# Performance work log

Measured on AMD Instinct MI355X. Metric: run time of the kernel, lower is better.

## Reference

```python
import jax, jax.numpy as jnp
import numpy as np

EMBED_DIM = 768
OUT_DIM = 768
EPS = 1e-06


def setup_inputs() -> dict:
    key = jax.random.key(0)
    ks = jax.random.split(key, 7)
    s_in = 1.0 / np.sqrt(EMBED_DIM)
    x = jax.random.normal(ks[0], (32, 1024, EMBED_DIM), dtype=jnp.float32)
    Wq = jax.random.normal(ks[1], (OUT_DIM, EMBED_DIM), dtype=jnp.float32) * s_in
    bq = jax.random.normal(ks[2], (OUT_DIM,), dtype=jnp.float32) * 0.01
    Wk = jax.random.normal(ks[3], (OUT_DIM, EMBED_DIM), dtype=jnp.float32) * s_in
    bk = jax.random.normal(ks[4], (OUT_DIM,), dtype=jnp.float32) * 0.01
    Wv = jax.random.normal(ks[5], (OUT_DIM, EMBED_DIM), dtype=jnp.float32) * s_in
    bv = jax.random.normal(ks[6], (OUT_DIM,), dtype=jnp.float32) * 0.01
    return {"x": x, "Wq": Wq, "bq": bq, "Wk": Wk, "bk": bk, "Wv": Wv, "bv": bv}


def reference(x, Wq, bq, Wk, bk, Wv, bv):
    # Q/K/V projections: nn.Linear computes x @ W.T + b
    Q = jnp.einsum('bnd,od->bno', x, Wq) + bq  # [B, N, O]
    K = jnp.einsum('bnd,od->bno', x, Wk) + bk
    V = jnp.einsum('bnd,od->bno', x, Wv) + bv
    scale = jnp.sqrt(jnp.asarray(OUT_DIM, dtype=x.dtype)) + EPS
    attn = jnp.einsum('bqo,bko->bqk', Q, K) / scale  # [B, N, N]
    weights = jax.nn.softmax(attn, axis=-1)
    # dropout p=0.0 -> identity (eval/inference)
    return jnp.einsum('bqk,bko->bqo', weights, V)
```

## Files before the change

kernel.cpp:

```cpp
#include <hip/hip_runtime.h>
#include <hip/hip_bf16.h>


typedef float  floatx4  __attribute__((ext_vector_type(4)));
typedef float  floatx16 __attribute__((ext_vector_type(16)));
typedef short  short8   __attribute__((ext_vector_type(8)));

__device__ __forceinline__ unsigned cvtpk(float lo, float hi) {
    unsigned r;
    asm("v_cvt_pk_bf16_f32 %0, %1, %2" : "=v"(r) : "v"(lo), "v"(hi));
    return r;
}
__device__ __forceinline__ floatx16 mfma32(short8 a, short8 b, floatx16 c) {
    return __builtin_amdgcn_mfma_f32_32x32x16_bf16(a, b, c, 0, 0, 0);
}
__device__ __forceinline__ void load_lds16(const void* g, void* lds) {
    __builtin_amdgcn_global_load_lds(
        (const __attribute__((address_space(1))) unsigned int*)g,
        (__attribute__((address_space(3))) unsigned int*)lds, 16, 0, 0);
}
__device__ __forceinline__ void bar_lds() {
    asm volatile("s_waitcnt lgkmcnt(0)" ::: "memory");
    __builtin_amdgcn_s_barrier();
    __builtin_amdgcn_sched_barrier(0);
}

__global__ __launch_bounds__(256) void cvt_bf16(
    const float* __restrict__ s0, unsigned short* __restrict__ d0, int n0,
    const float* __restrict__ s1, unsigned short* __restrict__ d1, int n1,
    const float* __restrict__ s2, unsigned short* __restrict__ d2, int n2,
    const float* __restrict__ s3, unsigned short* __restrict__ d3, int n3)
{
    const int stride = gridDim.x * blockDim.x;
    const int base   = blockIdx.x * blockDim.x + threadIdx.x;
    const float* ss[4] = {s0, s1, s2, s3};
    unsigned short* dd[4] = {d0, d1, d2, d3};
    const int nn[4] = {n0, n1, n2, n3};
#pragma unroll
    for (int j = 0; j < 4; ++j) {
        const floatx4* s = (const floatx4*)ss[j];
        uint4* d = (uint4*)dd[j];
        for (int i = base; i < nn[j]; i += stride) {
            floatx4 v0 = s[2 * i];
            floatx4 v1 = s[2 * i + 1];
            uint4 o;
            o.x = cvtpk(v0[0], v0[1]);
            o.y = cvtpk(v0[2], v0[3]);
            o.z = cvtpk(v1[0], v1[1]);
            o.w = cvtpk(v1[2], v1[3]);
            d[i] = o;
        }
    }
}

template <int MODE>
__global__ __launch_bounds__(256, 2) void gemm_lds(
    const unsigned short* __restrict__ A,
    const unsigned short* __restrict__ B,
    unsigned short* __restrict__ C, const float* __restrict__ bias,
    float alpha)
{
    __shared__ __align__(16) unsigned short As[2][128 * 64];
    __shared__ __align__(16) unsigned short Bs[2][128 * 64];

    const int tid = threadIdx.x;
    const int l   = tid & 63;
    const int w   = tid >> 6;
    const int wr  = w >> 1;
    const int wc  = w & 1;
    const int lo5 = l & 31;
    const int hi  = l >> 5;
    const int i0  = blockIdx.x * 128;
    const int j0  = blockIdx.y * 128;

    const int srow = l >> 3;
    const int sc16 = (l & 7) ^ srow;
    const unsigned short* Ag = A + (size_t)(i0 + srow) * 768 + sc16 * 8;
    const unsigned short* Bg = B + (size_t)(j0 + srow) * 768 + sc16 * 8;

    floatx16 acc[2][2] = {};

    auto STAGE = [&](int buf, int kt) {
        const int k0 = kt * 64;
#pragma unroll
        for (int t4 = 0; t4 < 4; ++t4) {
            const int t = w * 4 + t4;
            load_lds16(Ag + (size_t)t * 8 * 768 + k0, &As[buf][t * 512]);
            load_lds16(Bg + (size_t)t * 8 * 768 + k0, &Bs[buf][t * 512]);
        }
    };
    auto COMPUTE = [&](int buf) {
        const char* Ab = (const char*)As[buf];
        const char* Bb = (const char*)Bs[buf];
#pragma unroll
        for (int kk = 0; kk < 4; ++kk) {
            short8 a[2], b[2];
#pragma unroll
            for (int i = 0; i < 2; ++i) {
                const int r = wr * 64 + i * 32 + lo5;
                const unsigned off = r * 128 + ((unsigned)((kk * 2 + hi) ^ (r & 7)) << 4);
                a[i] = *reinterpret_cast<const short8*>(Ab + off);
            }
#pragma unroll
            for (int j = 0; j < 2; ++j) {
                const int r = wc * 64 + j * 32 + lo5;
                const unsigned off = r * 128 + ((unsigned)((kk * 2 + hi) ^ (r & 7)) << 4);
                b[j] = *reinterpret_cast<const short8*>(Bb + off);
            }
#pragma unroll
            for (int i = 0; i < 2; ++i)
#pragma unroll
                for (int j = 0; j < 2; ++j)
                    acc[i][j] = mfma32(a[i], b[j], acc[i][j]);
        }
    };

    STAGE(0, 0);
    __syncthreads();
#pragma unroll 1
    for (int kt = 0; kt < 12; ++kt) {
        if (kt + 1 < 12) STAGE((kt + 1) & 1, kt + 1);
        COMPUTE(kt & 1);
        __syncthreads();
    }

#pragma unroll
    for (int i = 0; i < 2; ++i) {
        float bvv[16];
        if (MODE == 0) {
#pragma unroll
            for (int r = 0; r < 16; ++r) {
                const int ol = (r & 3) + 8 * (r >> 2) + 4 * hi;
                bvv[r] = bias[i0 + wr * 64 + i * 32 + ol];
            }
        }
#pragma unroll
        for (int j = 0; j < 2; ++j) {
            float bj = 0.f;
            if (MODE == 1) bj = bias[j0 + wc * 64 + j * 32 + lo5];
            float v[16];
#pragma unroll
            for (int r = 0; r < 16; ++r)
                v[r] = (MODE == 0) ? (acc[i][j][r] + bvv[r]) * alpha
                                   : (acc[i][j][r] + bj);
#pragma unroll
            for (int cc = 0; cc < 2; ++cc) {
                unsigned w0 = cvtpk(v[8 * cc + 0], v[8 * cc + 1]);
                unsigned w1 = cvtpk(v[8 * cc + 2], v[8 * cc + 3]);
                unsigned w2 = cvtpk(v[8 * cc + 4], v[8 * cc + 5]);
                unsigned w3 = cvtpk(v[8 * cc + 6], v[8 * cc + 7]);
                unsigned x0 = __shfl_xor(w0, 32);
                unsigned x1 = __shfl_xor(w1, 32);
                unsigned x2 = __shfl_xor(w2, 32);
                unsigned x3 = __shfl_xor(w3, 32);
                uint4 st;
                st.x = hi ? x2 : w0;
                st.y = hi ? x3 : w1;
                st.z = hi ? w2 : x0;
                st.w = hi ? w3 : x1;
                size_t idx;
                if (MODE == 0) {
                    const int og = i0 + wr * 64 + i * 32 + cc * 16;
                    const int mg = j0 + wc * 64 + j * 32 + lo5;
                    idx = ((size_t)(mg >> 5) * 48 + (og >> 4)) * 512
                        + (size_t)(lo5 | (hi << 5)) * 8;
                } else {
                    const int ng = i0 + wr * 64 + i * 32 + cc * 16;
                    const int dg = j0 + wc * 64 + j * 32 + lo5;
                    idx = ((size_t)(ng >> 4) * 24 + (dg >> 5)) * 512
                        + (size_t)(lo5 | (hi << 5)) * 8;
                }
                *reinterpret_cast<uint4*>(C + idx) = st;
            }
        }
    }
}

__global__ __launch_bounds__(512, 1) void attn_kernel(
    const unsigned short* __restrict__ Qf,
    const unsigned short* __restrict__ Kf,
    const unsigned short* __restrict__ Vf,
    float* __restrict__ out)
{
    __shared__ __align__(16) unsigned short Q_lds[96 * 512];
    __shared__ __align__(16) unsigned short P_lds[32 * 512];

    const int tid = threadIdx.x;
    const int l   = tid & 63;
    const int w   = tid >> 6;
    const int lo5 = l & 31;
    const int hi  = l >> 5;

    const int bid = blockIdx.x;
    const int xcd = bid & 7;
    const int jj  = bid >> 3;
    const int b   = (jj >> 4) * 8 + xcd;
    const int qi  = jj & 15;
    const int q0  = qi * 64;

    const float MFIX = 12.0f;

    {
        const unsigned short* Qg = Qf + ((size_t)(b * 32 + qi * 2) * 48) * 512;
#pragma unroll
        for (int it = 0; it < 12; ++it) {
            const int t = w * 12 + it;
            const unsigned short* src = Qg + ((size_t)(t & 1) * 48 + (t >> 1)) * 512 + l * 8;
            load_lds16(src, &Q_lds[t * 512]);
        }
    }
    asm volatile("s_waitcnt vmcnt(0)" ::: "memory");
    __syncthreads();

    const short8* Kp = reinterpret_cast<const short8*>(Kf)
                       + ((size_t)b * 32 * 48) * 64 + l;
    const short8* Vp = reinterpret_cast<const short8*>(Vf)
                       + ((size_t)b * 64 * 24) * 64 + l;

    floatx16 acc[2][3] = {};
    float l_reg0 = 0.f, l_reg1 = 0.f;
    short8 vbuf[4][3];

#pragma unroll 1
    for (int c = 0; c < 4; ++c) {
        floatx16 s0 = {}, s1 = {};
        const short8* Kc = Kp + (size_t)(c * 8 + w) * 48 * 64;
        short8 kbuf[8];
#pragma unroll
        for (int u = 0; u < 8; ++u) kbuf[u] = Kc[(size_t)u * 64];
#pragma unroll 1
        for (int ks8 = 0; ks8 < 6; ++ks8) {
#pragma unroll
            for (int u = 0; u < 8; ++u) {
                const int ks = ks8 * 8 + u;
                short8 ka = kbuf[u];
                if (ks + 8 < 48) kbuf[u] = Kc[(size_t)(ks + 8) * 64];
                short8 qa0 = *reinterpret_cast<const short8*>(&Q_lds[((ks * 2 + 0) * 64 + l) * 8]);
                short8 qa1 = *reinterpret_cast<const short8*>(&Q_lds[((ks * 2 + 1) * 64 + l) * 8]);
                __builtin_amdgcn_s_setprio(1);
                s0 = mfma32(ka, qa0, s0);
                s1 = mfma32(ka, qa1, s1);
                __builtin_amdgcn_s_setprio(0);
            }
        }

        const short8* Vc = Vp + (size_t)(c * 16) * 24 * 64;
#pragma unroll
        for (int g = 0; g < 4; ++g)
#pragma unroll
            for (int jv = 0; jv < 3; ++jv)
                vbuf[g][jv] = Vc[((size_t)g * 24 + w * 3 + jv) * 64];

        float p0[16], p1[16];
        float sum0 = 0.f, sum1 = 0.f;
#pragma unroll
        for (int r = 0; r < 16; ++r) {
            p0[r] = __expf(s0[r] - MFIX); sum0 += p0[r];
            p1[r] = __expf(s1[r] - MFIX); sum1 += p1[r];
        }
        l_reg0 += sum0 + __shfl_xor(sum0, 32);
        l_reg1 += sum1 + __shfl_xor(sum1, 32);

        char* Pb = (char*)P_lds;
#pragma unroll
        for (int cc = 0; cc < 2; ++cc) {
#pragma unroll
            for (int jt = 0; jt < 2; ++jt) {
                const float* p = jt ? p1 : p0;
                unsigned w0 = cvtpk(p[8 * cc + 0], p[8 * cc + 1]);
                unsigned w1 = cvtpk(p[8 * cc + 2], p[8 * cc + 3]);
                unsigned w2 = cvtpk(p[8 * cc + 4], p[8 * cc + 5]);
                unsigned w3 = cvtpk(p[8 * cc + 6], p[8 * cc + 7]);
                unsigned x0 = __shfl_xor(w0, 32);
                unsigned x1 = __shfl_xor(w1, 32);
                unsigned x2 = __shfl_xor(w2, 32);
                unsigned x3 = __shfl_xor(w3, 32);
                uint4 st;
                st.x = hi ? x2 : w0;
                st.y = hi ? x3 : w1;
                st.z = hi ? w2 : x0;
                st.w = hi ? w3 : x1;
                const unsigned off = (((unsigned)(w * 2 + cc) * 2 + jt) * 64 + l) * 16;
                *reinterpret_cast<uint4*>(Pb + off) = st;
            }
        }
        bar_lds();

#pragma unroll
        for (int g = 0; g < 16; ++g) {
            short8 pa0 = *reinterpret_cast<const short8*>(&P_lds[((g * 2 + 0) * 64 + l) * 8]);
            short8 pa1 = *reinterpret_cast<const short8*>(&P_lds[((g * 2 + 1) * 64 + l) * 8]);
            short8 v0 = vbuf[g & 3][0];
            short8 v1 = vbuf[g & 3][1];
            short8 v2 = vbuf[g & 3][2];
            if (g < 12) {
#pragma unroll
                for (int jv = 0; jv < 3; ++jv)
                    vbuf[g & 3][jv] = Vc[((size_t)(g + 4) * 24 + w * 3 + jv) * 64];
            }
            __builtin_amdgcn_s_setprio(1);
            acc[0][0] = mfma32(pa0, v0, acc[0][0]);
            acc[1][0] = mfma32(pa1, v0, acc[1][0]);
            acc[0][1] = mfma32(pa0, v1, acc[0][1]);
            acc[1][1] = mfma32(pa1, v1, acc[1][1]);
            acc[0][2] = mfma32(pa0, v2, acc[0][2]);
            acc[1][2] = mfma32(pa1, v2, acc[1][2]);
            __builtin_amdgcn_s_setprio(0);
        }
        bar_lds();
    }

    float* lred = (float*)P_lds;
    if (hi == 0) {
        lred[(w * 2 + 0) * 32 + lo5] = l_reg0;
        lred[(w * 2 + 1) * 32 + lo5] = l_reg1;
    }
    bar_lds();
    float lt0 = 0.f, lt1 = 0.f;
#pragma unroll
    for (int wv = 0; wv < 8; ++wv) {
        lt0 += lred[(wv * 2 + 0) * 32 + lo5];
        lt1 += lred[(wv * 2 + 1) * 32 + lo5];
    }
    const float li0 = 1.0f / lt0;
    const float li1 = 1.0f / lt1;

#pragma unroll
    for (int jt = 0; jt < 2; ++jt)
#pragma unroll
        for (int r = 0; r < 16; ++r) {
            const int qr = (r & 3) + 8 * (r >> 2) + 4 * hi;
            const float linv = __shfl(jt ? li1 : li0, qr);
            const size_t grow = (size_t)(b * 1024 + q0 + jt * 32 + qr) * 768;
#pragma unroll
            for (int jv = 0; jv < 3; ++jv)
                out[grow + (w * 3 + jv) * 32 + lo5] = acc[jt][jv][r] * linv;
        }
}

extern "C" void kernel_launch(void* const* d_in, const int* in_sizes, int n_in,
                              void* d_out, int out_size, void* d_ws, size_t ws_size,
                              hipStream_t stream) {
    const float* x  = (const float*)d_in[0];
    const float* Wq = (const float*)d_in[1];
    const float* bq = (const float*)d_in[2];
    const float* Wk = (const float*)d_in[3];
    const float* bk = (const float*)d_in[4];
    const float* Wv = (const float*)d_in[5];
    const float* bv = (const float*)d_in[6];
    float* out = (float*)d_out;

    unsigned short* Qf = (unsigned short*)d_ws;
    unsigned short* Kf = Qf + 25165824u;
    unsigned short* Vf = Qf + 50331648u;

    unsigned short* xb  = (unsigned short*)d_out;
    unsigned short* Wqb = (unsigned short*)d_out + 25165824u;
    unsigned short* Wkb = Wqb + 589824u;
    unsigned short* Wvb = Wkb + 589824u;

    const float alpha_q = 1.0f / (sqrtf(768.0f) + 1e-6f);

    cvt_bf16<<<2048, 256, 0, stream>>>(x, xb, 3145728,
                                       Wq, Wqb, 73728,
                                       Wk, Wkb, 73728,
                                       Wv, Wvb, 73728);

    gemm_lds<0><<<dim3(6, 256), 256, 0, stream>>>(Wqb, xb, Qf, bq, alpha_q);
    gemm_lds<0><<<dim3(6, 256), 256, 0, stream>>>(Wkb, xb, Kf, bk, 1.0f);
    gemm_lds<1><<<dim3(256, 6), 256, 0, stream>>>(xb, Wvb, Vf, bv, 1.0f);

    attn_kernel<<<dim3(512), 512, 0, stream>>>(Qf, Kf, Vf, out);
}
```

Before: 333.4 us.

## Double-buffer P in LDS, prefetch next K chunk and LDS operands

Makes the P tile in LDS double-buffered so the barrier after the PV loop can be dropped, leaving one barrier per chunk. Prefetches the next chunk's K registers during the softmax phase, and software-pipelines the Q and P LDS reads one step ahead of the MFMAs. The goal is to hide global and LDS latency and cut synchronization. In exchange it uses more LDS and registers, and the row-sum reduction now reuses Q_lds after a final barrier.

```diff
diff --git a/kernel.cpp b/kernel.cpp
--- a/kernel.cpp
+++ b/kernel.cpp
@@ -183,7 +183,7 @@
     float* __restrict__ out)
 {
     __shared__ __align__(16) unsigned short Q_lds[96 * 512];
-    __shared__ __align__(16) unsigned short P_lds[32 * 512];
+    __shared__ __align__(16) unsigned short P_lds[2][32 * 512];
 
     const int tid = threadIdx.x;
     const int l   = tid & 63;
@@ -219,15 +219,20 @@
 
     floatx16 acc[2][3] = {};
     float l_reg0 = 0.f, l_reg1 = 0.f;
-    short8 vbuf[4][3];
+    short8 kbuf[8], vbuf[4][3];
+
+    {
+        const short8* Kc0 = Kp + (size_t)w * 48 * 64;
+#pragma unroll
+        for (int u = 0; u < 8; ++u) kbuf[u] = Kc0[(size_t)u * 64];
+    }
 
 #pragma unroll 1
     for (int c = 0; c < 4; ++c) {
         floatx16 s0 = {}, s1 = {};
         const short8* Kc = Kp + (size_t)(c * 8 + w) * 48 * 64;
-        short8 kbuf[8];
-#pragma unroll
-        for (int u = 0; u < 8; ++u) kbuf[u] = Kc[(size_t)u * 64];
+        short8 qa0 = *reinterpret_cast<const short8*>(&Q_lds[(0 * 64 + l) * 8]);
+        short8 qa1 = *reinterpret_cast<const short8*>(&Q_lds[(1 * 64 + l) * 8]);
 #pragma unroll 1
         for (int ks8 = 0; ks8 < 6; ++ks8) {
 #pragma unroll
@@ -235,12 +240,17 @@
                 const int ks = ks8 * 8 + u;
                 short8 ka = kbuf[u];
                 if (ks + 8 < 48) kbuf[u] = Kc[(size_t)(ks + 8) * 64];
-                short8 qa0 = *reinterpret_cast<const short8*>(&Q_lds[((ks * 2 + 0) * 64 + l) * 8]);
-                short8 qa1 = *reinterpret_cast<const short8*>(&Q_lds[((ks * 2 + 1) * 64 + l) * 8]);
+                short8 qn0, qn1;
+                if (ks + 1 < 48) {
+                    qn0 = *reinterpret_cast<const short8*>(&Q_lds[(((ks + 1) * 2 + 0) * 64 + l) * 8]);
+                    qn1 = *reinterpret_cast<const short8*>(&Q_lds[(((ks + 1) * 2 + 1) * 64 + l) * 8]);
+                }
                 __builtin_amdgcn_s_setprio(1);
                 s0 = mfma32(ka, qa0, s0);
                 s1 = mfma32(ka, qa1, s1);
                 __builtin_amdgcn_s_setprio(0);
+                qa0 = qn0;
+                qa1 = qn1;
             }
         }
 
@@ -250,6 +260,12 @@
 #pragma unroll
             for (int jv = 0; jv < 3; ++jv)
                 vbuf[g][jv] = Vc[((size_t)g * 24 + w * 3 + jv) * 64];
+
+        if (c < 3) {
+            const short8* Kn = Kp + (size_t)((c + 1) * 8 + w) * 48 * 64;
+#pragma unroll
+            for (int u = 0; u < 8; ++u) kbuf[u] = Kn[(size_t)u * 64];
+        }
 
         float p0[16], p1[16];
         float sum0 = 0.f, sum1 = 0.f;
@@ -261,7 +277,7 @@
         l_reg0 += sum0 + __shfl_xor(sum0, 32);
         l_reg1 += sum1 + __shfl_xor(sum1, 32);
 
-        char* Pb = (char*)P_lds;
+        char* Pb = (char*)P_lds[c & 1];
 #pragma unroll
         for (int cc = 0; cc < 2; ++cc) {
 #pragma unroll
@@ -286,10 +302,15 @@
         }
         bar_lds();
 
+        short8 pa0 = *reinterpret_cast<const short8*>(Pb + ((0 * 64 + l) * 16));
+        short8 pa1 = *reinterpret_cast<const short8*>(Pb + ((1 * 64 + l) * 16));
 #pragma unroll
         for (int g = 0; g < 16; ++g) {
-            short8 pa0 = *reinterpret_cast<const short8*>(&P_lds[((g * 2 + 0) * 64 + l) * 8]);
-            short8 pa1 = *reinterpret_cast<const short8*>(&P_lds[((g * 2 + 1) * 64 + l) * 8]);
+            short8 pn0, pn1;
+            if (g + 1 < 16) {
+                pn0 = *reinterpret_cast<const short8*>(Pb + ((((g + 1) * 2 + 0) * 64 + l) * 16));
+                pn1 = *reinterpret_cast<const short8*>(Pb + ((((g + 1) * 2 + 1) * 64 + l) * 16));
+            }
             short8 v0 = vbuf[g & 3][0];
             short8 v1 = vbuf[g & 3][1];
             short8 v2 = vbuf[g & 3][2];
@@ -306,11 +327,13 @@
             acc[0][2] = mfma32(pa0, v2, acc[0][2]);
             acc[1][2] = mfma32(pa1, v2, acc[1][2]);
             __builtin_amdgcn_s_setprio(0);
-        }
-        bar_lds();
-    }
-
-    float* lred = (float*)P_lds;
+            pa0 = pn0;
+            pa1 = pn1;
+        }
+    }
+
+    bar_lds();
+    float* lred = (float*)Q_lds;
     if (hi == 0) {
         lred[(w * 2 + 0) * 32 + lo5] = l_reg0;
         lred[(w * 2 + 1) * 32 + lo5] = l_reg1;
```

New measurement: 331.3 us. About the same (-0.6%).
